# Optimization experiments

Hardware: AMD Instinct MI355X
Metric: run time of the kernel (lower is better)

## Reference

```python
import jax, jax.numpy as jnp
import numpy as np

N_ATOMS = 200000
N_BONDS = 300000
E = 600000
D = 128
H = 128
EPS = 1e-5  # BatchNorm1d default eps


def setup_inputs() -> dict:
    key = jax.random.key(0)
    ks = jax.random.split(key, 8)
    x_atoms = jax.random.normal(ks[0], (N_ATOMS, D), jnp.float32)
    x_bonds = jax.random.normal(ks[1], (N_BONDS, D), jnp.float32)
    # atoms -> bonds edges: row0 src atom idx, row1 dst bond idx
    ei_ab = jnp.stack([
        jax.random.randint(ks[2], (E,), 0, N_ATOMS),
        jax.random.randint(ks[3], (E,), 0, N_BONDS),
    ]).astype(jnp.int64)
    # bonds -> atoms edges
    ei_ba = jnp.stack([
        jax.random.randint(ks[4], (E,), 0, N_BONDS),
        jax.random.randint(ks[5], (E,), 0, N_ATOMS),
    ]).astype(jnp.int64)
    xav = float(np.sqrt(6.0 / (D + H)))
    W = jax.random.uniform(ks[6], (H, D), jnp.float32, -xav, xav)   # shared lin_rel
    b = jnp.zeros((H,), jnp.float32)
    Wr = jax.random.uniform(ks[7], (H, D), jnp.float32, -xav, xav)  # res_connection
    br = jnp.zeros((H,), jnp.float32)
    return {
        "x_atoms": x_atoms, "x_bonds": x_bonds,
        "ei_ab": ei_ab, "ei_ba": ei_ba,
        "W": W, "b": b, "Wr": Wr, "br": br,
        "gamma_atoms": jnp.ones((H,), jnp.float32),
        "beta_atoms": jnp.zeros((H,), jnp.float32),
        "gamma_bonds": jnp.ones((H,), jnp.float32),
        "beta_bonds": jnp.zeros((H,), jnp.float32),
    }


def _bn(v, g, bt):
    # BatchNorm1d training-mode math: batch mean, biased variance
    m = v.mean(axis=0)
    var = v.var(axis=0)
    return (v - m) * jax.lax.rsqrt(var + EPS) * g + bt


def reference(x_atoms, x_bonds, ei_ab, ei_ba, W, b, Wr, br,
              gamma_atoms, beta_atoms, gamma_bonds, beta_bonds):
    # shared lin_rel applied to both node types
    h_atoms = x_atoms @ W.T + b   # [N_ATOMS, H]
    h_bonds = x_bonds @ W.T + b   # [N_BONDS, H]

    # message = lin(x_src)[src], aggregate = scatter-add at dst (source_to_target)
    agg_bonds = jax.ops.segment_sum(h_atoms[ei_ab[0]], ei_ab[1], num_segments=N_BONDS)
    agg_atoms = jax.ops.segment_sum(h_bonds[ei_ba[0]], ei_ba[1], num_segments=N_ATOMS)

    # residual: activation(res_connection(x))
    out_atoms = agg_atoms + jax.nn.relu(x_atoms @ Wr.T + br)
    out_bonds = agg_bonds + jax.nn.relu(x_bonds @ Wr.T + br)

    # dropout is identity in eval/deterministic reference
    out_atoms = _bn(out_atoms, gamma_atoms, beta_atoms)
    out_bonds = _bn(out_bonds, gamma_bonds, beta_bonds)
    return out_atoms, out_bonds
```

## Files before the change

kernel.cpp:

```cpp
#include <hip/hip_runtime.h>
#include <stdint.h>

#define NATOMS 200000
#define NBONDS 300000
#define NEDGE  600000
#define NSEG   (NATOMS + NBONDS)
#define DF     128
#define EPS    1e-5f
#define SCHUNK 2048
#define NSBLK  ((NSEG + SCHUNK - 1) / SCHUNK)
#define NCHA   (NATOMS / 64)
#define NCHB   ((NBONDS + 63) / 64)
#define NCH    (NCHA + NCHB)
#define NBUCK  32

typedef __attribute__((ext_vector_type(8))) short bf16x8;
typedef __attribute__((ext_vector_type(4))) float f32x4;
typedef unsigned short u16;
typedef __attribute__((ext_vector_type(4))) unsigned short u16x4;

__device__ __forceinline__ short f2b(float f) {
  union { float f; uint32_t u; } v; v.f = f;
  uint32_t r = v.u + 0x7fffu + ((v.u >> 16) & 1u);
  return (short)(r >> 16);
}
__device__ __forceinline__ float bf2f(u16 h) {
  union { uint32_t u; float f; } v; v.u = ((uint32_t)h) << 16; return v.f;
}
__device__ __forceinline__ bf16x8 pack8(float4 u, float4 v) {
  bf16x8 t;
  t[0] = f2b(u.x); t[1] = f2b(u.y); t[2] = f2b(u.z); t[3] = f2b(u.w);
  t[4] = f2b(v.x); t[5] = f2b(v.y); t[6] = f2b(v.z); t[7] = f2b(v.w);
  return t;
}

__global__ void k_prep(const float* __restrict__ W, const float* __restrict__ Wr,
                       u16* __restrict__ Wb, u16* __restrict__ Wrb) {
  int i = blockIdx.x * blockDim.x + threadIdx.x;
  if (i < DF * DF) {
    Wb[i]  = (u16)f2b(W[i]);
    Wrb[i] = (u16)f2b(Wr[i]);
  }
}

__global__ void k_conv(const float* __restrict__ x, u16* __restrict__ xT, int n8) {
  int stride = gridDim.x * blockDim.x;
  for (int i = blockIdx.x * blockDim.x + threadIdx.x; i < n8; i += stride) {
    const float4 a = *(const float4*)(x + (size_t)i * 8);
    const float4 b = *(const float4*)(x + (size_t)i * 8 + 4);
    *(bf16x8*)(xT + (size_t)i * 8) = pack8(a, b);
  }
}

__global__ void k_hist(const int* __restrict__ ab, const int* __restrict__ ba,
                       int* __restrict__ cnt) {
  int stride = gridDim.x * blockDim.x;
  for (int e = blockIdx.x * blockDim.x + threadIdx.x; e < 2 * NEDGE; e += stride) {
    int g;
    if (e < NEDGE) g = NATOMS + ab[NEDGE + e];
    else           g = ba[NEDGE + (e - NEDGE)];
    atomicAdd(cnt + g, 1);
  }
}

__global__ void k_scanA(const int* __restrict__ cnt, int* __restrict__ bsum) {
  __shared__ int wsm[4];
  int t = threadIdx.x;
  int base = blockIdx.x * SCHUNK + t * 8;
  int s = 0;
#pragma unroll
  for (int j = 0; j < 8; ++j) { int i = base + j; if (i < NSEG) s += cnt[i]; }
  for (int d = 1; d < 64; d <<= 1) s += __shfl_xor(s, d);
  if ((t & 63) == 0) wsm[t >> 6] = s;
  __syncthreads();
  if (t == 0) bsum[blockIdx.x] = wsm[0] + wsm[1] + wsm[2] + wsm[3];
}

__global__ void k_scanB(const int* __restrict__ bsum, int* __restrict__ bbase) {
  __shared__ int wsm[4];
  int t = threadIdx.x;
  int lane = t & 63;
  int v = (t < NSBLK) ? bsum[t] : 0;
  int s = v;
  for (int d = 1; d < 64; d <<= 1) { int n = __shfl_up(s, d); if (lane >= d) s += n; }
  if (lane == 63) wsm[t >> 6] = s;
  __syncthreads();
  int wbase = 0;
  for (int w = 0; w < (t >> 6); ++w) wbase += wsm[w];
  if (t < NSBLK) bbase[t] = wbase + s - v;
}

__global__ void k_scanC(const int* __restrict__ cnt, const int* __restrict__ bbase,
                        int* __restrict__ off, int* __restrict__ cursor) {
  __shared__ int wsm[4];
  int t = threadIdx.x;
  int lane = t & 63, wv = t >> 6;
  int base = blockIdx.x * SCHUNK + t * 8;
  int v[8]; int ts = 0;
#pragma unroll
  for (int j = 0; j < 8; ++j) { int i = base + j; v[j] = (i < NSEG) ? cnt[i] : 0; ts += v[j]; }
  int s = ts;
  for (int d = 1; d < 64; d <<= 1) { int n = __shfl_up(s, d); if (lane >= d) s += n; }
  if (lane == 63) wsm[wv] = s;
  __syncthreads();
  int wbase = bbase[blockIdx.x];
  for (int w = 0; w < wv; ++w) wbase += wsm[w];
  int run = wbase + s - ts;
#pragma unroll
  for (int j = 0; j < 8; ++j) {
    int i = base + j;
    if (i < NSEG) { off[i] = run; cursor[i] = run; }
    run += v[j];
  }
}

__global__ void k_fill(const int* __restrict__ ab, const int* __restrict__ ba,
                       int* __restrict__ cursor, int* __restrict__ sorted) {
  int stride = gridDim.x * blockDim.x;
  for (int e = blockIdx.x * blockDim.x + threadIdx.x; e < 2 * NEDGE; e += stride) {
    int g, src;
    if (e < NEDGE) { g = NATOMS + ab[NEDGE + e]; src = ab[e]; }
    else { int e2 = e - NEDGE; g = ba[NEDGE + e2]; src = ba[e2]; }
    int pos = atomicAdd(cursor + g, 1);
    sorted[pos] = src;
  }
}

template<int AGG, int XT>
__global__ void k_gather(const float* __restrict__ xa, const float* __restrict__ xb,
                         const u16* __restrict__ xaT, const u16* __restrict__ xbT,
                         const int* __restrict__ sorted, const int* __restrict__ off,
                         const int* __restrict__ cnt,
                         float* __restrict__ outf, u16* __restrict__ aggT) {
  int l32 = threadIdx.x & 31;
  int hwid = (blockIdx.x * blockDim.x + threadIdx.x) >> 5;
  int nhw = (gridDim.x * blockDim.x) >> 5;
  for (int g = hwid; g < NSEG; g += nhw) {
    int start = off[g], deg = cnt[g];
    float a0 = 0.f, a1 = 0.f, a2 = 0.f, a3 = 0.f;
    if constexpr (XT) {
      const u16* src = (g < NATOMS) ? xbT : xaT;
      int k = 0;
      for (; k + 1 < deg; k += 2) {
        int s0 = sorted[start + k], s1 = sorted[start + k + 1];
        u16x4 v0 = *(const u16x4*)(src + (size_t)s0 * DF + l32 * 4);
        u16x4 v1 = *(const u16x4*)(src + (size_t)s1 * DF + l32 * 4);
        a0 += bf2f(v0[0]) + bf2f(v1[0]);
        a1 += bf2f(v0[1]) + bf2f(v1[1]);
        a2 += bf2f(v0[2]) + bf2f(v1[2]);
        a3 += bf2f(v0[3]) + bf2f(v1[3]);
      }
      if (k < deg) {
        int s0 = sorted[start + k];
        u16x4 v0 = *(const u16x4*)(src + (size_t)s0 * DF + l32 * 4);
        a0 += bf2f(v0[0]); a1 += bf2f(v0[1]); a2 += bf2f(v0[2]); a3 += bf2f(v0[3]);
      }
    } else {
      const float* src = (g < NATOMS) ? xb : xa;
      int k = 0;
      for (; k + 1 < deg; k += 2) {
        int s0 = sorted[start + k], s1 = sorted[start + k + 1];
        float4 v0 = *(const float4*)(src + (size_t)s0 * DF + l32 * 4);
        float4 v1 = *(const float4*)(src + (size_t)s1 * DF + l32 * 4);
        a0 += v0.x + v1.x; a1 += v0.y + v1.y; a2 += v0.z + v1.z; a3 += v0.w + v1.w;
      }
      if (k < deg) {
        int s0 = sorted[start + k];
        float4 v0 = *(const float4*)(src + (size_t)s0 * DF + l32 * 4);
        a0 += v0.x; a1 += v0.y; a2 += v0.z; a3 += v0.w;
      }
    }
    if constexpr (AGG) {
      u16x4 r;
      r[0] = (u16)f2b(a0); r[1] = (u16)f2b(a1); r[2] = (u16)f2b(a2); r[3] = (u16)f2b(a3);
      *(u16x4*)(aggT + (size_t)g * DF + l32 * 4) = r;
    } else {
      float4 r; r.x = a0; r.y = a1; r.z = a2; r.w = a3;
      *(float4*)(outf + (size_t)g * DF + l32 * 4) = r;
    }
  }
}

template<int AGG, int XT>
__global__ __launch_bounds__(256, 3) void k_gemm(
    const float* __restrict__ xa, const float* __restrict__ xb,
    const u16* __restrict__ xaT, const u16* __restrict__ xbT,
    const u16* __restrict__ aggT, float* __restrict__ outf,
    const int* __restrict__ cnt,
    const u16* __restrict__ Wb, const u16* __restrict__ Wrb,
    const float* __restrict__ bb, const float* __restrict__ brb,
    float* __restrict__ stats) {
  int lane = threadIdx.x & 63;
  int wv = threadIdx.x >> 6;
  int r16 = lane & 15, kq = lane >> 4;
  int t0 = wv * 2;

  bf16x8 wf[2][4], wrf[2][4];
#pragma unroll
  for (int ti = 0; ti < 2; ++ti) {
#pragma unroll
    for (int kk = 0; kk < 4; ++kk) {
      size_t o = (size_t)((t0 + ti) * 16 + r16) * DF + kk * 32 + kq * 8;
      wf[ti][kk]  = *(const bf16x8*)(Wb + o);
      wrf[ti][kk] = *(const bf16x8*)(Wrb + o);
    }
  }
  float bvv[2], brr[2];
#pragma unroll
  for (int ti = 0; ti < 2; ++ti) {
    bvv[ti] = bb[(t0 + ti) * 16 + r16];
    brr[ti] = brb[(t0 + ti) * 16 + r16];
  }

  float sA[2] = {0.f, 0.f}, qA[2] = {0.f, 0.f};
  float sB[2] = {0.f, 0.f}, qB[2] = {0.f, 0.f};

  for (int c = blockIdx.x; c < NCH; c += gridDim.x) {
    int typ, nrows, goff, base;
    if (c < NCHA) { typ = 0; nrows = NATOMS; goff = 0; base = c * 64; }
    else { typ = 1; nrows = NBONDS; goff = NATOMS; base = (c - NCHA) * 64; }
    const float* xsrc = typ ? xb : xa;
    const u16* xsrcT = typ ? xbT : xaT;

#pragma unroll
    for (int rg = 0; rg < 4; ++rg) {
      int rowbase = base + rg * 16;
      if (rowbase < nrows) {
        int row = rowbase + r16;
        bf16x8 fA[4], fX[4];
        if constexpr (AGG) {
          const u16* ap = aggT + (size_t)(goff + row) * DF + kq * 8;
#pragma unroll
          for (int kk = 0; kk < 4; ++kk) fA[kk] = *(const bf16x8*)(ap + kk * 32);
        } else {
          const float* ap = outf + (size_t)(goff + row) * DF + kq * 8;
#pragma unroll
          for (int kk = 0; kk < 4; ++kk)
            fA[kk] = pack8(*(const float4*)(ap + kk * 32),
                           *(const float4*)(ap + kk * 32 + 4));
        }
        if constexpr (XT) {
          const u16* xp = xsrcT + (size_t)row * DF + kq * 8;
#pragma unroll
          for (int kk = 0; kk < 4; ++kk) fX[kk] = *(const bf16x8*)(xp + kk * 32);
        } else {
          const float* xp = xsrc + (size_t)row * DF + kq * 8;
#pragma unroll
          for (int kk = 0; kk < 4; ++kk)
            fX[kk] = pack8(*(const float4*)(xp + kk * 32),
                           *(const float4*)(xp + kk * 32 + 4));
        }

        f32x4 accW[2], accR[2];
#pragma unroll
        for (int ti = 0; ti < 2; ++ti) {
#pragma unroll
          for (int r = 0; r < 4; ++r) { accW[ti][r] = 0.f; accR[ti][r] = 0.f; }
        }
#pragma unroll
        for (int kk = 0; kk < 4; ++kk) {
#pragma unroll
          for (int ti = 0; ti < 2; ++ti) {
            accW[ti] = __builtin_amdgcn_mfma_f32_16x16x32_bf16(fA[kk], wf[ti][kk], accW[ti], 0, 0, 0);
            accR[ti] = __builtin_amdgcn_mfma_f32_16x16x32_bf16(fX[kk], wrf[ti][kk], accR[ti], 0, 0, 0);
          }
        }

        float cf[4];
#pragma unroll
        for (int r = 0; r < 4; ++r)
          cf[r] = (float)cnt[goff + rowbase + kq * 4 + r];

#pragma unroll
        for (int ti = 0; ti < 2; ++ti) {
          int feat = (t0 + ti) * 16 + r16;
          float s = 0.f, q = 0.f;
#pragma unroll
          for (int r = 0; r < 4; ++r) {
            int grow = rowbase + kq * 4 + r;
            float g = accW[ti][r] + cf[r] * bvv[ti] + fmaxf(accR[ti][r] + brr[ti], 0.f);
            outf[(size_t)(goff + grow) * DF + feat] = g;
            s += g; q += g * g;
          }
          if (typ == 0) { sA[ti] += s; qA[ti] += q; }
          else          { sB[ti] += s; qB[ti] += q; }
        }
      }
    }
  }

  int bkt = blockIdx.x & (NBUCK - 1);
#pragma unroll
  for (int ti = 0; ti < 2; ++ti) {
    float s0 = sA[ti], q0 = qA[ti], s1 = sB[ti], q1 = qB[ti];
    s0 += __shfl_xor(s0, 16); q0 += __shfl_xor(q0, 16);
    s1 += __shfl_xor(s1, 16); q1 += __shfl_xor(q1, 16);
    s0 += __shfl_xor(s0, 32); q0 += __shfl_xor(q0, 32);
    s1 += __shfl_xor(s1, 32); q1 += __shfl_xor(q1, 32);
    if (kq == 0) {
      int feat = (t0 + ti) * 16 + r16;
      float* p = stats + (size_t)bkt * 4 * DF;
      atomicAdd(p + 0 * DF + feat, s0);
      atomicAdd(p + 1 * DF + feat, q0);
      atomicAdd(p + 2 * DF + feat, s1);
      atomicAdd(p + 3 * DF + feat, q1);
    }
  }
}

__global__ void k_stats(const float* __restrict__ stats,
                        const float* __restrict__ ga, const float* __restrict__ bea,
                        const float* __restrict__ gb, const float* __restrict__ beb,
                        float* __restrict__ scale, float* __restrict__ shift) {
  int tid = threadIdx.x;
  if (tid < 2 * DF) {
    int t = tid >> 7, f = tid & (DF - 1);
    float S = 0.f, SS = 0.f;
    for (int bk = 0; bk < NBUCK; ++bk) {
      const float* p = stats + (size_t)bk * 4 * DF;
      S  += p[(2 * t) * DF + f];
      SS += p[(2 * t + 1) * DF + f];
    }
    float n = t ? (float)NBONDS : (float)NATOMS;
    float mean = S / n;
    float var = SS / n - mean * mean;
    float rstd = rsqrtf(var + EPS);
    float g = t ? gb[f] : ga[f];
    float be = t ? beb[f] : bea[f];
    scale[tid] = rstd * g;
    shift[tid] = be - mean * rstd * g;
  }
}

__global__ void k_norm(float* __restrict__ out, const float* __restrict__ scale,
                       const float* __restrict__ shift) {
  const size_t nv = (size_t)NSEG * DF / 4;
  size_t stride = (size_t)gridDim.x * blockDim.x;
  for (size_t i = (size_t)blockIdx.x * blockDim.x + threadIdx.x; i < nv; i += stride) {
    size_t e = i * 4;
    int t = e >= (size_t)NATOMS * DF;
    int f = (int)(e & (DF - 1));
    const float* sc = scale + t * DF + f;
    const float* sh = shift + t * DF + f;
    float4 v = ((float4*)out)[i];
    v.x = fmaf(v.x, sc[0], sh[0]);
    v.y = fmaf(v.y, sc[1], sh[1]);
    v.z = fmaf(v.z, sc[2], sh[2]);
    v.w = fmaf(v.w, sc[3], sh[3]);
    ((float4*)out)[i] = v;
  }
}

extern "C" void kernel_launch(void* const* d_in, const int* in_sizes, int n_in,
                              void* d_out, int out_size, void* d_ws, size_t ws_size,
                              hipStream_t stream) {
  const float* xa  = (const float*)d_in[0];
  const float* xb  = (const float*)d_in[1];
  const int*   ab  = (const int*)d_in[2];
  const int*   ba  = (const int*)d_in[3];
  const float* W   = (const float*)d_in[4];
  const float* b   = (const float*)d_in[5];
  const float* Wr  = (const float*)d_in[6];
  const float* br  = (const float*)d_in[7];
  const float* ga  = (const float*)d_in[8];
  const float* bea = (const float*)d_in[9];
  const float* gb  = (const float*)d_in[10];
  const float* beb = (const float*)d_in[11];
  float* out = (float*)d_out;

  char* ws = (char*)d_ws;
  int*   cnt    = (int*)ws;
  int*   off    = (int*)(ws +  2000000);
  int*   cursor = (int*)(ws +  4000000);
  int*   sorted = (int*)(ws +  6000000);
  float* stats  = (float*)(ws + 10800000);
  int*   bsum   = (int*)(ws + 10865536);
  int*   bbase  = (int*)(ws + 10866560);
  u16*   Wbf    = (u16*)(ws + 10867584);
  u16*   Wrbf   = (u16*)(ws + 10900352);
  float* scale  = (float*)(ws + 10933120);
  float* shift  = (float*)(ws + 10934144);
  u16*   aggT = (u16*)(ws + 10935168);
  u16*   xaT  = (u16*)(ws + 138935168);
  u16*   xbT  = (u16*)(ws + 190135168);
  const bool agg = ws_size >= 138935168ull;
  const bool xt  = ws_size >= 266935168ull;

  hipMemsetAsync(cnt, 0, 2000000, stream);
  hipMemsetAsync(stats, 0, 65536, stream);

  k_prep<<<64, 256, 0, stream>>>(W, Wr, Wbf, Wrbf);
  if (xt) {
    k_conv<<<2048, 256, 0, stream>>>(xa, xaT, NATOMS * DF / 8);
    k_conv<<<2048, 256, 0, stream>>>(xb, xbT, NBONDS * DF / 8);
  }
  k_hist<<<2048, 256, 0, stream>>>(ab, ba, cnt);
  k_scanA<<<NSBLK, 256, 0, stream>>>(cnt, bsum);
  k_scanB<<<1, 256, 0, stream>>>(bsum, bbase);
  k_scanC<<<NSBLK, 256, 0, stream>>>(cnt, bbase, off, cursor);
  k_fill<<<2048, 256, 0, stream>>>(ab, ba, cursor, sorted);

  if (xt) {
    k_gather<1, 1><<<4096, 256, 0, stream>>>(xa, xb, xaT, xbT, sorted, off, cnt, out, aggT);
    k_gemm<1, 1><<<2048, 256, 0, stream>>>(xa, xb, xaT, xbT, aggT, out, cnt,
                                           Wbf, Wrbf, b, br, stats);
  } else if (agg) {
    k_gather<1, 0><<<4096, 256, 0, stream>>>(xa, xb, xaT, xbT, sorted, off, cnt, out, aggT);
    k_gemm<1, 0><<<2048, 256, 0, stream>>>(xa, xb, xaT, xbT, aggT, out, cnt,
                                           Wbf, Wrbf, b, br, stats);
  } else {
    k_gather<0, 0><<<4096, 256, 0, stream>>>(xa, xb, xaT, xbT, sorted, off, cnt, out, aggT);
    k_gemm<0, 0><<<2048, 256, 0, stream>>>(xa, xb, xaT, xbT, aggT, out, cnt,
                                           Wbf, Wrbf, b, br, stats);
  }
  k_stats<<<1, 256, 0, stream>>>(stats, ga, bea, gb, beb, scale, shift);
  k_norm<<<8192, 256, 0, stream>>>(out, scale, shift);
}
```

Baseline: 611.8 us.

## Fuse BatchNorm apply into a second GEMM pass and widen the gather

The separate normalization pass is removed. The GEMM now runs twice: a first pass only accumulates per-feature sum and sum of squares, and a second pass recomputes the GEMM and writes the already normalized output using the scale and shift from k_stats. This drops one full write and one full read of the fp32 output in exchange for reading the bf16 aggregates and inputs twice and doing the MFMA work twice. The bf16 gather is also rewritten so that each full wave handles one segment, with four edges in flight and 16-byte loads, followed by a shuffle reduction. The GEMM grid becomes one 64-row chunk per block, and the middle workspace tier is dropped.

```diff
diff --git a/kernel.cpp b/kernel.cpp
--- a/kernel.cpp
+++ b/kernel.cpp
@@ -126,62 +126,67 @@
   }
 }
 
-template<int AGG, int XT>
-__global__ void k_gather(const float* __restrict__ xa, const float* __restrict__ xb,
-                         const u16* __restrict__ xaT, const u16* __restrict__ xbT,
-                         const int* __restrict__ sorted, const int* __restrict__ off,
-                         const int* __restrict__ cnt,
-                         float* __restrict__ outf, u16* __restrict__ aggT) {
+__global__ void k_gather_b(const u16* __restrict__ xaT, const u16* __restrict__ xbT,
+                           const int* __restrict__ sorted, const int* __restrict__ off,
+                           const int* __restrict__ cnt, u16* __restrict__ aggT) {
+  int lane = threadIdx.x & 63;
+  int l16 = lane & 15, e4 = lane >> 4;
+  int wid = (blockIdx.x * blockDim.x + threadIdx.x) >> 6;
+  int nw = (gridDim.x * blockDim.x) >> 6;
+  for (int g = wid; g < NSEG; g += nw) {
+    int start = off[g], deg = cnt[g];
+    const u16* src = (g < NATOMS) ? xbT : xaT;
+    float acc[8];
+#pragma unroll
+    for (int j = 0; j < 8; ++j) acc[j] = 0.f;
+    for (int k = e4; k < deg; k += 4) {
+      int s = sorted[start + k];
+      bf16x8 v = *(const bf16x8*)(src + (size_t)s * DF + l16 * 8);
+#pragma unroll
+      for (int j = 0; j < 8; ++j) acc[j] += bf2f((u16)v[j]);
+    }
+#pragma unroll
+    for (int j = 0; j < 8; ++j) {
+      acc[j] += __shfl_xor(acc[j], 16);
+      acc[j] += __shfl_xor(acc[j], 32);
+    }
+    if (e4 == 0) {
+      bf16x8 r;
+#pragma unroll
+      for (int j = 0; j < 8; ++j) r[j] = f2b(acc[j]);
+      *(bf16x8*)(aggT + (size_t)g * DF + l16 * 8) = r;
+    }
+  }
+}
+
+__global__ void k_gather_f(const float* __restrict__ xa, const float* __restrict__ xb,
+                           const int* __restrict__ sorted, const int* __restrict__ off,
+                           const int* __restrict__ cnt, float* __restrict__ outf) {
   int l32 = threadIdx.x & 31;
   int hwid = (blockIdx.x * blockDim.x + threadIdx.x) >> 5;
   int nhw = (gridDim.x * blockDim.x) >> 5;
   for (int g = hwid; g < NSEG; g += nhw) {
     int start = off[g], deg = cnt[g];
+    const float* src = (g < NATOMS) ? xb : xa;
     float a0 = 0.f, a1 = 0.f, a2 = 0.f, a3 = 0.f;
-    if constexpr (XT) {
-      const u16* src = (g < NATOMS) ? xbT : xaT;
-      int k = 0;
-      for (; k + 1 < deg; k += 2) {
-        int s0 = sorted[start + k], s1 = sorted[start + k + 1];
-        u16x4 v0 = *(const u16x4*)(src + (size_t)s0 * DF + l32 * 4);
-        u16x4 v1 = *(const u16x4*)(src + (size_t)s1 * DF + l32 * 4);
-        a0 += bf2f(v0[0]) + bf2f(v1[0]);
-        a1 += bf2f(v0[1]) + bf2f(v1[1]);
-        a2 += bf2f(v0[2]) + bf2f(v1[2]);
-        a3 += bf2f(v0[3]) + bf2f(v1[3]);
-      }
-      if (k < deg) {
-        int s0 = sorted[start + k];
-        u16x4 v0 = *(const u16x4*)(src + (size_t)s0 * DF + l32 * 4);
-        a0 += bf2f(v0[0]); a1 += bf2f(v0[1]); a2 += bf2f(v0[2]); a3 += bf2f(v0[3]);
-      }
-    } else {
-      const float* src = (g < NATOMS) ? xb : xa;
-      int k = 0;
-      for (; k + 1 < deg; k += 2) {
-        int s0 = sorted[start + k], s1 = sorted[start + k + 1];
-        float4 v0 = *(const float4*)(src + (size_t)s0 * DF + l32 * 4);
-        float4 v1 = *(const float4*)(src + (size_t)s1 * DF + l32 * 4);
-        a0 += v0.x + v1.x; a1 += v0.y + v1.y; a2 += v0.z + v1.z; a3 += v0.w + v1.w;
-      }
-      if (k < deg) {
-        int s0 = sorted[start + k];
-        float4 v0 = *(const float4*)(src + (size_t)s0 * DF + l32 * 4);
-        a0 += v0.x; a1 += v0.y; a2 += v0.z; a3 += v0.w;
-      }
-    }
-    if constexpr (AGG) {
-      u16x4 r;
-      r[0] = (u16)f2b(a0); r[1] = (u16)f2b(a1); r[2] = (u16)f2b(a2); r[3] = (u16)f2b(a3);
-      *(u16x4*)(aggT + (size_t)g * DF + l32 * 4) = r;
-    } else {
-      float4 r; r.x = a0; r.y = a1; r.z = a2; r.w = a3;
-      *(float4*)(outf + (size_t)g * DF + l32 * 4) = r;
-    }
-  }
-}
-
-template<int AGG, int XT>
+    int k = 0;
+    for (; k + 1 < deg; k += 2) {
+      int s0 = sorted[start + k], s1 = sorted[start + k + 1];
+      float4 v0 = *(const float4*)(src + (size_t)s0 * DF + l32 * 4);
+      float4 v1 = *(const float4*)(src + (size_t)s1 * DF + l32 * 4);
+      a0 += v0.x + v1.x; a1 += v0.y + v1.y; a2 += v0.z + v1.z; a3 += v0.w + v1.w;
+    }
+    if (k < deg) {
+      int s0 = sorted[start + k];
+      float4 v0 = *(const float4*)(src + (size_t)s0 * DF + l32 * 4);
+      a0 += v0.x; a1 += v0.y; a2 += v0.z; a3 += v0.w;
+    }
+    float4 r; r.x = a0; r.y = a1; r.z = a2; r.w = a3;
+    *(float4*)(outf + (size_t)g * DF + l32 * 4) = r;
+  }
+}
+
+template<int PHASE, int TIER>
 __global__ __launch_bounds__(256, 3) void k_gemm(
     const float* __restrict__ xa, const float* __restrict__ xb,
     const u16* __restrict__ xaT, const u16* __restrict__ xbT,
@@ -189,7 +194,8 @@
     const int* __restrict__ cnt,
     const u16* __restrict__ Wb, const u16* __restrict__ Wrb,
     const float* __restrict__ bb, const float* __restrict__ brb,
-    float* __restrict__ stats) {
+    float* __restrict__ stats,
+    const float* __restrict__ scale, const float* __restrict__ shift) {
   int lane = threadIdx.x & 63;
   int wv = threadIdx.x >> 6;
   int r16 = lane & 15, kq = lane >> 4;
@@ -212,98 +218,103 @@
     brr[ti] = brb[(t0 + ti) * 16 + r16];
   }
 
-  float sA[2] = {0.f, 0.f}, qA[2] = {0.f, 0.f};
-  float sB[2] = {0.f, 0.f}, qB[2] = {0.f, 0.f};
-
-  for (int c = blockIdx.x; c < NCH; c += gridDim.x) {
-    int typ, nrows, goff, base;
-    if (c < NCHA) { typ = 0; nrows = NATOMS; goff = 0; base = c * 64; }
-    else { typ = 1; nrows = NBONDS; goff = NATOMS; base = (c - NCHA) * 64; }
-    const float* xsrc = typ ? xb : xa;
-    const u16* xsrcT = typ ? xbT : xaT;
-
-#pragma unroll
-    for (int rg = 0; rg < 4; ++rg) {
-      int rowbase = base + rg * 16;
-      if (rowbase < nrows) {
-        int row = rowbase + r16;
-        bf16x8 fA[4], fX[4];
-        if constexpr (AGG) {
-          const u16* ap = aggT + (size_t)(goff + row) * DF + kq * 8;
-#pragma unroll
-          for (int kk = 0; kk < 4; ++kk) fA[kk] = *(const bf16x8*)(ap + kk * 32);
-        } else {
-          const float* ap = outf + (size_t)(goff + row) * DF + kq * 8;
-#pragma unroll
-          for (int kk = 0; kk < 4; ++kk)
-            fA[kk] = pack8(*(const float4*)(ap + kk * 32),
-                           *(const float4*)(ap + kk * 32 + 4));
+  int c = blockIdx.x;
+  int typ, nrows, goff, base;
+  if (c < NCHA) { typ = 0; nrows = NATOMS; goff = 0; base = c * 64; }
+  else { typ = 1; nrows = NBONDS; goff = NATOMS; base = (c - NCHA) * 64; }
+  const float* xsrc = typ ? xb : xa;
+  const u16* xsrcT = typ ? xbT : xaT;
+
+  float sc2[2], sh2[2];
+  if constexpr (PHASE == 1) {
+#pragma unroll
+    for (int ti = 0; ti < 2; ++ti) {
+      int feat = (t0 + ti) * 16 + r16;
+      sc2[ti] = scale[typ * DF + feat];
+      sh2[ti] = shift[typ * DF + feat];
+    }
+  }
+
+  float sacc[2] = {0.f, 0.f}, qacc[2] = {0.f, 0.f};
+
+#pragma unroll
+  for (int rg = 0; rg < 4; ++rg) {
+    int rowbase = base + rg * 16;
+    if (rowbase < nrows) {
+      int row = rowbase + r16;
+      bf16x8 fA[4], fX[4];
+      if constexpr (TIER) {
+        const u16* ap = aggT + (size_t)(goff + row) * DF + kq * 8;
+        const u16* xp = xsrcT + (size_t)row * DF + kq * 8;
+#pragma unroll
+        for (int kk = 0; kk < 4; ++kk) {
+          fA[kk] = *(const bf16x8*)(ap + kk * 32);
+          fX[kk] = *(const bf16x8*)(xp + kk * 32);
         }
-        if constexpr (XT) {
-          const u16* xp = xsrcT + (size_t)row * DF + kq * 8;
-#pragma unroll
-          for (int kk = 0; kk < 4; ++kk) fX[kk] = *(const bf16x8*)(xp + kk * 32);
-        } else {
-          const float* xp = xsrc + (size_t)row * DF + kq * 8;
-#pragma unroll
-          for (int kk = 0; kk < 4; ++kk)
-            fX[kk] = pack8(*(const float4*)(xp + kk * 32),
-                           *(const float4*)(xp + kk * 32 + 4));
+      } else {
+        const float* ap = outf + (size_t)(goff + row) * DF + kq * 8;
+        const float* xp = xsrc + (size_t)row * DF + kq * 8;
+#pragma unroll
+        for (int kk = 0; kk < 4; ++kk) {
+          fA[kk] = pack8(*(const float4*)(ap + kk * 32),
+                         *(const float4*)(ap + kk * 32 + 4));
+          fX[kk] = pack8(*(const float4*)(xp + kk * 32),
+                         *(const float4*)(xp + kk * 32 + 4));
         }
-
-        f32x4 accW[2], accR[2];
+      }
+
+      f32x4 accW[2], accR[2];
+#pragma unroll
+      for (int ti = 0; ti < 2; ++ti) {
+#pragma unroll
+        for (int r = 0; r < 4; ++r) { accW[ti][r] = 0.f; accR[ti][r] = 0.f; }
+      }
+#pragma unroll
+      for (int kk = 0; kk < 4; ++kk) {
 #pragma unroll
         for (int ti = 0; ti < 2; ++ti) {
-#pragma unroll
-          for (int r = 0; r < 4; ++r) { accW[ti][r] = 0.f; accR[ti][r] = 0.f; }
+          accW[ti] = __builtin_amdgcn_mfma_f32_16x16x32_bf16(fA[kk], wf[ti][kk], accW[ti], 0, 0, 0);
+          accR[ti] = __builtin_amdgcn_mfma_f32_16x16x32_bf16(fX[kk], wrf[ti][kk], accR[ti], 0, 0, 0);
         }
-#pragma unroll
-        for (int kk = 0; kk < 4; ++kk) {
-#pragma unroll
-          for (int ti = 0; ti < 2; ++ti) {
-            accW[ti] = __builtin_amdgcn_mfma_f32_16x16x32_bf16(fA[kk], wf[ti][kk], accW[ti], 0, 0, 0);
-            accR[ti] = __builtin_amdgcn_mfma_f32_16x16x32_bf16(fX[kk], wrf[ti][kk], accR[ti], 0, 0, 0);
+      }
+
+      float cf[4];
+#pragma unroll
+      for (int r = 0; r < 4; ++r)
+        cf[r] = (float)cnt[goff + rowbase + kq * 4 + r];
+
+#pragma unroll
+      for (int ti = 0; ti < 2; ++ti) {
+        int feat = (t0 + ti) * 16 + r16;
+        float s = 0.f, q = 0.f;
+#pragma unroll
+        for (int r = 0; r < 4; ++r) {
+          int grow = rowbase + kq * 4 + r;
+          float g = accW[ti][r] + cf[r] * bvv[ti] + fmaxf(accR[ti][r] + brr[ti], 0.f);
+          if constexpr (PHASE == 0) {
+            s += g; q += g * g;
+          } else {
+            outf[(size_t)(goff + grow) * DF + feat] = fmaf(g, sc2[ti], sh2[ti]);
           }
         }
-
-        float cf[4];
-#pragma unroll
-        for (int r = 0; r < 4; ++r)
-          cf[r] = (float)cnt[goff + rowbase + kq * 4 + r];
-
-#pragma unroll
-        for (int ti = 0; ti < 2; ++ti) {
-          int feat = (t0 + ti) * 16 + r16;
-          float s = 0.f, q = 0.f;
-#pragma unroll
-          for (int r = 0; r < 4; ++r) {
-            int grow = rowbase + kq * 4 + r;
-            float g = accW[ti][r] + cf[r] * bvv[ti] + fmaxf(accR[ti][r] + brr[ti], 0.f);
-            outf[(size_t)(goff + grow) * DF + feat] = g;
-            s += g; q += g * g;
-          }
-          if (typ == 0) { sA[ti] += s; qA[ti] += q; }
-          else          { sB[ti] += s; qB[ti] += q; }
-        }
+        if constexpr (PHASE == 0) { sacc[ti] += s; qacc[ti] += q; }
       }
     }
   }
 
-  int bkt = blockIdx.x & (NBUCK - 1);
-#pragma unroll
-  for (int ti = 0; ti < 2; ++ti) {
-    float s0 = sA[ti], q0 = qA[ti], s1 = sB[ti], q1 = qB[ti];
-    s0 += __shfl_xor(s0, 16); q0 += __shfl_xor(q0, 16);
-    s1 += __shfl_xor(s1, 16); q1 += __shfl_xor(q1, 16);
-    s0 += __shfl_xor(s0, 32); q0 += __shfl_xor(q0, 32);
-    s1 += __shfl_xor(s1, 32); q1 += __shfl_xor(q1, 32);
-    if (kq == 0) {
-      int feat = (t0 + ti) * 16 + r16;
-      float* p = stats + (size_t)bkt * 4 * DF;
-      atomicAdd(p + 0 * DF + feat, s0);
-      atomicAdd(p + 1 * DF + feat, q0);
-      atomicAdd(p + 2 * DF + feat, s1);
-      atomicAdd(p + 3 * DF + feat, q1);
+  if constexpr (PHASE == 0) {
+    int bkt = blockIdx.x & (NBUCK - 1);
+    float* p = stats + (size_t)bkt * 4 * DF + typ * 2 * DF;
+#pragma unroll
+    for (int ti = 0; ti < 2; ++ti) {
+      float s = sacc[ti], q = qacc[ti];
+      s += __shfl_xor(s, 16); q += __shfl_xor(q, 16);
+      s += __shfl_xor(s, 32); q += __shfl_xor(q, 32);
+      if (kq == 0) {
+        int feat = (t0 + ti) * 16 + r16;
+        atomicAdd(p + feat, s);
+        atomicAdd(p + DF + feat, q);
+      }
     }
   }
 }
@@ -329,25 +340,6 @@
     float be = t ? beb[f] : bea[f];
     scale[tid] = rstd * g;
     shift[tid] = be - mean * rstd * g;
-  }
-}
-
-__global__ void k_norm(float* __restrict__ out, const float* __restrict__ scale,
-                       const float* __restrict__ shift) {
-  const size_t nv = (size_t)NSEG * DF / 4;
-  size_t stride = (size_t)gridDim.x * blockDim.x;
-  for (size_t i = (size_t)blockIdx.x * blockDim.x + threadIdx.x; i < nv; i += stride) {
-    size_t e = i * 4;
-    int t = e >= (size_t)NATOMS * DF;
-    int f = (int)(e & (DF - 1));
-    const float* sc = scale + t * DF + f;
-    const float* sh = shift + t * DF + f;
-    float4 v = ((float4*)out)[i];
-    v.x = fmaf(v.x, sc[0], sh[0]);
-    v.y = fmaf(v.y, sc[1], sh[1]);
-    v.z = fmaf(v.z, sc[2], sh[2]);
-    v.w = fmaf(v.w, sc[3], sh[3]);
-    ((float4*)out)[i] = v;
   }
 }
 
@@ -383,8 +375,7 @@
   u16*   aggT = (u16*)(ws + 10935168);
   u16*   xaT  = (u16*)(ws + 138935168);
   u16*   xbT  = (u16*)(ws + 190135168);
-  const bool agg = ws_size >= 138935168ull;
-  const bool xt  = ws_size >= 266935168ull;
+  const bool xt = ws_size >= 266935168ull;
 
   hipMemsetAsync(cnt, 0, 2000000, stream);
   hipMemsetAsync(stats, 0, 65536, stream);
@@ -401,18 +392,18 @@
   k_fill<<<2048, 256, 0, stream>>>(ab, ba, cursor, sorted);
 
   if (xt) {
-    k_gather<1, 1><<<4096, 256, 0, stream>>>(xa, xb, xaT, xbT, sorted, off, cnt, out, aggT);
-    k_gemm<1, 1><<<2048, 256, 0, stream>>>(xa, xb, xaT, xbT, aggT, out, cnt,
-                                           Wbf, Wrbf, b, br, stats);
-  } else if (agg) {
-    k_gather<1, 0><<<4096, 256, 0, stream>>>(xa, xb, xaT, xbT, sorted, off, cnt, out, aggT);
-    k_gemm<1, 0><<<2048, 256, 0, stream>>>(xa, xb, xaT, xbT, aggT, out, cnt,
-                                           Wbf, Wrbf, b, br, stats);
+    k_gather_b<<<8192, 256, 0, stream>>>(xaT, xbT, sorted, off, cnt, aggT);
+    k_gemm<0, 1><<<NCH, 256, 0, stream>>>(xa, xb, xaT, xbT, aggT, out, cnt,
+                                          Wbf, Wrbf, b, br, stats, scale, shift);
+    k_stats<<<1, 256, 0, stream>>>(stats, ga, bea, gb, beb, scale, shift);
+    k_gemm<1, 1><<<NCH, 256, 0, stream>>>(xa, xb, xaT, xbT, aggT, out, cnt,
+                                          Wbf, Wrbf, b, br, stats, scale, shift);
   } else {
-    k_gather<0, 0><<<4096, 256, 0, stream>>>(xa, xb, xaT, xbT, sorted, off, cnt, out, aggT);
-    k_gemm<0, 0><<<2048, 256, 0, stream>>>(xa, xb, xaT, xbT, aggT, out, cnt,
-                                           Wbf, Wrbf, b, br, stats);
-  }
-  k_stats<<<1, 256, 0, stream>>>(stats, ga, bea, gb, beb, scale, shift);
-  k_norm<<<8192, 256, 0, stream>>>(out, scale, shift);
-}
+    k_gather_f<<<8192, 256, 0, stream>>>(xa, xb, sorted, off, cnt, out);
+    k_gemm<0, 0><<<NCH, 256, 0, stream>>>(xa, xb, xaT, xbT, aggT, out, cnt,
+                                          Wbf, Wrbf, b, br, stats, scale, shift);
+    k_stats<<<1, 256, 0, stream>>>(stats, ga, bea, gb, beb, scale, shift);
+    k_gemm<1, 0><<<NCH, 256, 0, stream>>>(xa, xb, xaT, xbT, aggT, out, cnt,
+                                          Wbf, Wrbf, b, br, stats, scale, shift);
+  }
+}
```

After: 758.0 us. 23.9% more time.

## Fuse edge gather into GEMM and store pre-norm output as bf16

Applied to the files above, without the earlier changes.

In the bf16 path, the GEMM kernel now gathers and sums neighbor rows itself for each tile row, so the separate gather kernel and its aggregate buffer round-trip go away. The pre-normalization result is written as bf16 into a scratch buffer, and the norm kernel reads bf16 and writes fp32, which halves that intermediate traffic. Launch bounds drop to 2 waves per SIMD, the grid grows, and the fp32 fallback path gains a barrier. The cost is per-lane serial gathers inside the MFMA kernel, which may be latency bound, plus extra bf16 rounding on the output.

```diff
diff --git a/kernel.cpp b/kernel.cpp
--- a/kernel.cpp
+++ b/kernel.cpp
@@ -17,7 +17,6 @@
 typedef __attribute__((ext_vector_type(8))) short bf16x8;
 typedef __attribute__((ext_vector_type(4))) float f32x4;
 typedef unsigned short u16;
-typedef __attribute__((ext_vector_type(4))) unsigned short u16x4;
 
 __device__ __forceinline__ short f2b(float f) {
   union { float f; uint32_t u; } v; v.f = f;
@@ -126,66 +125,39 @@
   }
 }
 
-template<int AGG, int XT>
-__global__ void k_gather(const float* __restrict__ xa, const float* __restrict__ xb,
-                         const u16* __restrict__ xaT, const u16* __restrict__ xbT,
-                         const int* __restrict__ sorted, const int* __restrict__ off,
-                         const int* __restrict__ cnt,
-                         float* __restrict__ outf, u16* __restrict__ aggT) {
+__global__ void k_gather_f(const float* __restrict__ xa, const float* __restrict__ xb,
+                           const int* __restrict__ sorted, const int* __restrict__ off,
+                           const int* __restrict__ cnt, float* __restrict__ outf) {
   int l32 = threadIdx.x & 31;
   int hwid = (blockIdx.x * blockDim.x + threadIdx.x) >> 5;
   int nhw = (gridDim.x * blockDim.x) >> 5;
   for (int g = hwid; g < NSEG; g += nhw) {
     int start = off[g], deg = cnt[g];
+    const float* src = (g < NATOMS) ? xb : xa;
     float a0 = 0.f, a1 = 0.f, a2 = 0.f, a3 = 0.f;
-    if constexpr (XT) {
-      const u16* src = (g < NATOMS) ? xbT : xaT;
-      int k = 0;
-      for (; k + 1 < deg; k += 2) {
-        int s0 = sorted[start + k], s1 = sorted[start + k + 1];
-        u16x4 v0 = *(const u16x4*)(src + (size_t)s0 * DF + l32 * 4);
-        u16x4 v1 = *(const u16x4*)(src + (size_t)s1 * DF + l32 * 4);
-        a0 += bf2f(v0[0]) + bf2f(v1[0]);
-        a1 += bf2f(v0[1]) + bf2f(v1[1]);
-        a2 += bf2f(v0[2]) + bf2f(v1[2]);
-        a3 += bf2f(v0[3]) + bf2f(v1[3]);
-      }
-      if (k < deg) {
-        int s0 = sorted[start + k];
-        u16x4 v0 = *(const u16x4*)(src + (size_t)s0 * DF + l32 * 4);
-        a0 += bf2f(v0[0]); a1 += bf2f(v0[1]); a2 += bf2f(v0[2]); a3 += bf2f(v0[3]);
-      }
-    } else {
-      const float* src = (g < NATOMS) ? xb : xa;
-      int k = 0;
-      for (; k + 1 < deg; k += 2) {
-        int s0 = sorted[start + k], s1 = sorted[start + k + 1];
-        float4 v0 = *(const float4*)(src + (size_t)s0 * DF + l32 * 4);
-        float4 v1 = *(const float4*)(src + (size_t)s1 * DF + l32 * 4);
-        a0 += v0.x + v1.x; a1 += v0.y + v1.y; a2 += v0.z + v1.z; a3 += v0.w + v1.w;
-      }
-      if (k < deg) {
-        int s0 = sorted[start + k];
-        float4 v0 = *(const float4*)(src + (size_t)s0 * DF + l32 * 4);
-        a0 += v0.x; a1 += v0.y; a2 += v0.z; a3 += v0.w;
-      }
-    }
-    if constexpr (AGG) {
-      u16x4 r;
-      r[0] = (u16)f2b(a0); r[1] = (u16)f2b(a1); r[2] = (u16)f2b(a2); r[3] = (u16)f2b(a3);
-      *(u16x4*)(aggT + (size_t)g * DF + l32 * 4) = r;
-    } else {
-      float4 r; r.x = a0; r.y = a1; r.z = a2; r.w = a3;
-      *(float4*)(outf + (size_t)g * DF + l32 * 4) = r;
-    }
-  }
-}
-
-template<int AGG, int XT>
-__global__ __launch_bounds__(256, 3) void k_gemm(
+    int k = 0;
+    for (; k + 1 < deg; k += 2) {
+      int s0 = sorted[start + k], s1 = sorted[start + k + 1];
+      float4 v0 = *(const float4*)(src + (size_t)s0 * DF + l32 * 4);
+      float4 v1 = *(const float4*)(src + (size_t)s1 * DF + l32 * 4);
+      a0 += v0.x + v1.x; a1 += v0.y + v1.y; a2 += v0.z + v1.z; a3 += v0.w + v1.w;
+    }
+    if (k < deg) {
+      int s0 = sorted[start + k];
+      float4 v0 = *(const float4*)(src + (size_t)s0 * DF + l32 * 4);
+      a0 += v0.x; a1 += v0.y; a2 += v0.z; a3 += v0.w;
+    }
+    float4 r; r.x = a0; r.y = a1; r.z = a2; r.w = a3;
+    *(float4*)(outf + (size_t)g * DF + l32 * 4) = r;
+  }
+}
+
+template<int TIER>
+__global__ __launch_bounds__(256, 2) void k_gemm(
     const float* __restrict__ xa, const float* __restrict__ xb,
     const u16* __restrict__ xaT, const u16* __restrict__ xbT,
-    const u16* __restrict__ aggT, float* __restrict__ outf,
+    const int* __restrict__ sorted, const int* __restrict__ off,
+    float* __restrict__ outf, u16* __restrict__ gT,
     const int* __restrict__ cnt,
     const u16* __restrict__ Wb, const u16* __restrict__ Wrb,
     const float* __restrict__ bb, const float* __restrict__ brb,
@@ -219,36 +191,63 @@
     int typ, nrows, goff, base;
     if (c < NCHA) { typ = 0; nrows = NATOMS; goff = 0; base = c * 64; }
     else { typ = 1; nrows = NBONDS; goff = NATOMS; base = (c - NCHA) * 64; }
-    const float* xsrc = typ ? xb : xa;
-    const u16* xsrcT = typ ? xbT : xaT;
 
 #pragma unroll
     for (int rg = 0; rg < 4; ++rg) {
       int rowbase = base + rg * 16;
       if (rowbase < nrows) {
         int row = rowbase + r16;
-        bf16x8 fA[4], fX[4];
-        if constexpr (AGG) {
-          const u16* ap = aggT + (size_t)(goff + row) * DF + kq * 8;
-#pragma unroll
-          for (int kk = 0; kk < 4; ++kk) fA[kk] = *(const bf16x8*)(ap + kk * 32);
-        } else {
-          const float* ap = outf + (size_t)(goff + row) * DF + kq * 8;
-#pragma unroll
-          for (int kk = 0; kk < 4; ++kk)
-            fA[kk] = pack8(*(const float4*)(ap + kk * 32),
-                           *(const float4*)(ap + kk * 32 + 4));
-        }
-        if constexpr (XT) {
-          const u16* xp = xsrcT + (size_t)row * DF + kq * 8;
+        int gidx = goff + row;
+
+        bf16x8 fX[4];
+        if constexpr (TIER) {
+          const u16* xp = (typ ? xbT : xaT) + (size_t)row * DF + kq * 8;
 #pragma unroll
           for (int kk = 0; kk < 4; ++kk) fX[kk] = *(const bf16x8*)(xp + kk * 32);
         } else {
-          const float* xp = xsrc + (size_t)row * DF + kq * 8;
+          const float* xp = (typ ? xb : xa) + (size_t)row * DF + kq * 8;
 #pragma unroll
           for (int kk = 0; kk < 4; ++kk)
             fX[kk] = pack8(*(const float4*)(xp + kk * 32),
                            *(const float4*)(xp + kk * 32 + 4));
+        }
+
+        float a0[8], a1[8], a2[8], a3[8];
+        if constexpr (TIER) {
+#pragma unroll
+          for (int j = 0; j < 8; ++j) { a0[j] = 0.f; a1[j] = 0.f; a2[j] = 0.f; a3[j] = 0.f; }
+          int start = off[gidx], deg = cnt[gidx];
+          const u16* gsrc = typ ? xaT : xbT;
+          for (int k = 0; k < deg; ++k) {
+            int s = sorted[start + k];
+            const u16* p = gsrc + (size_t)s * DF + kq * 8;
+            bf16x8 v0 = *(const bf16x8*)(p);
+            bf16x8 v1 = *(const bf16x8*)(p + 32);
+            bf16x8 v2 = *(const bf16x8*)(p + 64);
+            bf16x8 v3 = *(const bf16x8*)(p + 96);
+#pragma unroll
+            for (int j = 0; j < 8; ++j) {
+              a0[j] += bf2f((u16)v0[j]); a1[j] += bf2f((u16)v1[j]);
+              a2[j] += bf2f((u16)v2[j]); a3[j] += bf2f((u16)v3[j]);
+            }
+          }
+        } else {
+          const float* ap = outf + (size_t)gidx * DF + kq * 8;
+#pragma unroll
+          for (int j = 0; j < 8; ++j) {
+            a0[j] = ap[j]; a1[j] = ap[32 + j]; a2[j] = ap[64 + j]; a3[j] = ap[96 + j];
+          }
+        }
+
+        bf16x8 fA[4];
+#pragma unroll
+        for (int j = 0; j < 8; ++j) {
+          fA[0][j] = f2b(a0[j]); fA[1][j] = f2b(a1[j]);
+          fA[2][j] = f2b(a2[j]); fA[3][j] = f2b(a3[j]);
+        }
+
+        if constexpr (!TIER) {
+          __syncthreads();
         }
 
         f32x4 accW[2], accR[2];
@@ -279,7 +278,8 @@
           for (int r = 0; r < 4; ++r) {
             int grow = rowbase + kq * 4 + r;
             float g = accW[ti][r] + cf[r] * bvv[ti] + fmaxf(accR[ti][r] + brr[ti], 0.f);
-            outf[(size_t)(goff + grow) * DF + feat] = g;
+            if constexpr (TIER) gT[(size_t)(goff + grow) * DF + feat] = (u16)f2b(g);
+            else                outf[(size_t)(goff + grow) * DF + feat] = g;
             s += g; q += g * g;
           }
           if (typ == 0) { sA[ti] += s; qA[ti] += q; }
@@ -290,6 +290,7 @@
   }
 
   int bkt = blockIdx.x & (NBUCK - 1);
+  float* p = stats + (size_t)bkt * 4 * DF;
 #pragma unroll
   for (int ti = 0; ti < 2; ++ti) {
     float s0 = sA[ti], q0 = qA[ti], s1 = sB[ti], q1 = qB[ti];
@@ -299,7 +300,6 @@
     s1 += __shfl_xor(s1, 32); q1 += __shfl_xor(q1, 32);
     if (kq == 0) {
       int feat = (t0 + ti) * 16 + r16;
-      float* p = stats + (size_t)bkt * 4 * DF;
       atomicAdd(p + 0 * DF + feat, s0);
       atomicAdd(p + 1 * DF + feat, q0);
       atomicAdd(p + 2 * DF + feat, s1);
@@ -332,22 +332,47 @@
   }
 }
 
-__global__ void k_norm(float* __restrict__ out, const float* __restrict__ scale,
-                       const float* __restrict__ shift) {
-  const size_t nv = (size_t)NSEG * DF / 4;
-  size_t stride = (size_t)gridDim.x * blockDim.x;
-  for (size_t i = (size_t)blockIdx.x * blockDim.x + threadIdx.x; i < nv; i += stride) {
-    size_t e = i * 4;
-    int t = e >= (size_t)NATOMS * DF;
-    int f = (int)(e & (DF - 1));
-    const float* sc = scale + t * DF + f;
-    const float* sh = shift + t * DF + f;
-    float4 v = ((float4*)out)[i];
-    v.x = fmaf(v.x, sc[0], sh[0]);
-    v.y = fmaf(v.y, sc[1], sh[1]);
-    v.z = fmaf(v.z, sc[2], sh[2]);
-    v.w = fmaf(v.w, sc[3], sh[3]);
-    ((float4*)out)[i] = v;
+template<int TIER>
+__global__ void k_norm(float* __restrict__ out, const u16* __restrict__ gT,
+                       const float* __restrict__ scale, const float* __restrict__ shift) {
+  if constexpr (TIER) {
+    const size_t nv = (size_t)NSEG * DF / 8;
+    size_t stride = (size_t)gridDim.x * blockDim.x;
+    for (size_t i = (size_t)blockIdx.x * blockDim.x + threadIdx.x; i < nv; i += stride) {
+      size_t e = i * 8;
+      int t = e >= (size_t)NATOMS * DF;
+      int f = (int)(e & (DF - 1));
+      bf16x8 v = *(const bf16x8*)(gT + e);
+      const float* sc = scale + t * DF + f;
+      const float* sh = shift + t * DF + f;
+      float4 o0, o1;
+      o0.x = fmaf(bf2f((u16)v[0]), sc[0], sh[0]);
+      o0.y = fmaf(bf2f((u16)v[1]), sc[1], sh[1]);
+      o0.z = fmaf(bf2f((u16)v[2]), sc[2], sh[2]);
+      o0.w = fmaf(bf2f((u16)v[3]), sc[3], sh[3]);
+      o1.x = fmaf(bf2f((u16)v[4]), sc[4], sh[4]);
+      o1.y = fmaf(bf2f((u16)v[5]), sc[5], sh[5]);
+      o1.z = fmaf(bf2f((u16)v[6]), sc[6], sh[6]);
+      o1.w = fmaf(bf2f((u16)v[7]), sc[7], sh[7]);
+      *(float4*)(out + e) = o0;
+      *(float4*)(out + e + 4) = o1;
+    }
+  } else {
+    const size_t nv = (size_t)NSEG * DF / 4;
+    size_t stride = (size_t)gridDim.x * blockDim.x;
+    for (size_t i = (size_t)blockIdx.x * blockDim.x + threadIdx.x; i < nv; i += stride) {
+      size_t e = i * 4;
+      int t = e >= (size_t)NATOMS * DF;
+      int f = (int)(e & (DF - 1));
+      const float* sc = scale + t * DF + f;
+      const float* sh = shift + t * DF + f;
+      float4 v = ((float4*)out)[i];
+      v.x = fmaf(v.x, sc[0], sh[0]);
+      v.y = fmaf(v.y, sc[1], sh[1]);
+      v.z = fmaf(v.z, sc[2], sh[2]);
+      v.w = fmaf(v.w, sc[3], sh[3]);
+      ((float4*)out)[i] = v;
+    }
   }
 }
 
@@ -380,11 +405,10 @@
   u16*   Wrbf   = (u16*)(ws + 10900352);
   float* scale  = (float*)(ws + 10933120);
   float* shift  = (float*)(ws + 10934144);
-  u16*   aggT = (u16*)(ws + 10935168);
+  u16*   gT   = (u16*)(ws + 10935168);
   u16*   xaT  = (u16*)(ws + 138935168);
   u16*   xbT  = (u16*)(ws + 190135168);
-  const bool agg = ws_size >= 138935168ull;
-  const bool xt  = ws_size >= 266935168ull;
+  const bool xt = ws_size >= 266935168ull;
 
   hipMemsetAsync(cnt, 0, 2000000, stream);
   hipMemsetAsync(stats, 0, 65536, stream);
@@ -401,18 +425,15 @@
   k_fill<<<2048, 256, 0, stream>>>(ab, ba, cursor, sorted);
 
   if (xt) {
-    k_gather<1, 1><<<4096, 256, 0, stream>>>(xa, xb, xaT, xbT, sorted, off, cnt, out, aggT);
-    k_gemm<1, 1><<<2048, 256, 0, stream>>>(xa, xb, xaT, xbT, aggT, out, cnt,
-                                           Wbf, Wrbf, b, br, stats);
-  } else if (agg) {
-    k_gather<1, 0><<<4096, 256, 0, stream>>>(xa, xb, xaT, xbT, sorted, off, cnt, out, aggT);
-    k_gemm<1, 0><<<2048, 256, 0, stream>>>(xa, xb, xaT, xbT, aggT, out, cnt,
-                                           Wbf, Wrbf, b, br, stats);
+    k_gemm<1><<<4096, 256, 0, stream>>>(xa, xb, xaT, xbT, sorted, off, out, gT, cnt,
+                                        Wbf, Wrbf, b, br, stats);
+    k_stats<<<1, 256, 0, stream>>>(stats, ga, bea, gb, beb, scale, shift);
+    k_norm<1><<<4096, 256, 0, stream>>>(out, gT, scale, shift);
   } else {
-    k_gather<0, 0><<<4096, 256, 0, stream>>>(xa, xb, xaT, xbT, sorted, off, cnt, out, aggT);
-    k_gemm<0, 0><<<2048, 256, 0, stream>>>(xa, xb, xaT, xbT, aggT, out, cnt,
-                                           Wbf, Wrbf, b, br, stats);
-  }
-  k_stats<<<1, 256, 0, stream>>>(stats, ga, bea, gb, beb, scale, shift);
-  k_norm<<<8192, 256, 0, stream>>>(out, scale, shift);
-}
+    k_gather_f<<<8192, 256, 0, stream>>>(xa, xb, sorted, off, cnt, out);
+    k_gemm<0><<<4096, 256, 0, stream>>>(xa, xb, xaT, xbT, sorted, off, out, gT, cnt,
+                                        Wbf, Wrbf, b, br, stats);
+    k_stats<<<1, 256, 0, stream>>>(stats, ga, bea, gb, beb, scale, shift);
+    k_norm<0><<<8192, 256, 0, stream>>>(out, gT, scale, shift);
+  }
+}
```

After: 677.3 us. 1.11x slower.
